# Performance work log

Hardware: AMD Instinct MI355X
Metric: run time of the kernel (lower is better)

Reference implementation:

```python
import jax, jax.numpy as jnp
import numpy as np

VALUE_DIM = 512
VALUE_SIZE = 262144
NUM_LABELS = 64
C = 256
B, T = 4, 1024


def setup_inputs() -> dict:
    key = jax.random.key(0)
    k1, k2, k3, k4, k5 = jax.random.split(key, 5)
    indices = jax.random.randint(k1, (B, T), 0, VALUE_SIZE, dtype=jnp.int64 if jax.config.jax_enable_x64 else jnp.int32)
    scores = jax.random.normal(k2, (B, T), dtype=jnp.float32)
    W = jax.random.normal(k3, (NUM_LABELS, VALUE_DIM, C), dtype=jnp.float32)
    label = jax.random.randint(k4, (B, T), 0, NUM_LABELS, dtype=jnp.int32)
    weight = jax.random.normal(k5, (VALUE_SIZE, VALUE_DIM), dtype=jnp.float32)
    return {"indices": indices, "scores": scores, "W": W, "label": label, "index": 1, "weight": weight}


def reference(indices, scores, W, label, index, weight):
    half = VALUE_DIM // 2
    if index == 1:
        weight_h = weight[:, half:]          # (V, half)
        W_h = W[:, half:, :]                 # (L, half, C)
    else:
        weight_h = weight[:, :half]
        W_h = W[:, :half, :]
    # gather embeddings: (b, t, half)
    selected_values = weight_h[indices]
    # label-indexed matrix gather: (b, t, half, C)
    expanded_params = W_h[label]
    # fused batched matvec + score weighting + sum over t -> (b, C)
    out = jnp.einsum('btd,btdc,bt->bc', selected_values, expanded_params, scores)
    return out
```

## Files before the change

kernel.cpp:

```cpp
#include <hip/hip_runtime.h>

#define Bdim   4
#define Tdim   1024
#define NLAB   64
#define Cdim   256
#define Ddim   512
#define HALF   256
#define BT     (Bdim*Tdim)

__global__ __launch_bounds__(256) void vb_kernel(
    const int*   __restrict__ indices,
    const float* __restrict__ scores,
    const float* __restrict__ W,
    const int*   __restrict__ label,
    const int*   __restrict__ index_p,
    const float* __restrict__ weight,
    float*       __restrict__ out)
{
    const int l     = blockIdx.x & 63;
    const int chunk = blockIdx.x >> 6;
    const int tid   = threadIdx.x;
    const int half  = (index_p[0] == 1) ? HALF : 0;
    const int dglob = half + chunk * 64;

    __shared__ int   s_list[BT];
    __shared__ int   s_count;
    __shared__ float A_part[4][Bdim][64];
    __shared__ float A_red[Bdim][64];
    __shared__ float P[4][Bdim][Cdim];

    if (tid == 0) s_count = 0;
    {
        float* ap = &A_part[0][0][0];
        #pragma unroll
        for (int i = 0; i < 4; ++i) ap[tid + 256 * i] = 0.0f;
    }
    __syncthreads();

    #pragma unroll
    for (int i = 0; i < BT / 256; ++i) {
        int bt = i * 256 + tid;
        if (label[bt] == l) {
            int pos = atomicAdd(&s_count, 1);
            s_list[pos] = bt;
        }
    }
    __syncthreads();
    const int count = s_count;

    const int slot = tid >> 6;
    const int dl   = tid & 63;
    for (int m = slot; m < count; m += 4) {
        int   bt  = s_list[m];
        int   b   = bt >> 10;
        float s   = scores[bt];
        int   idx = indices[bt];
        float w   = weight[(size_t)idx * Ddim + dglob + dl];
        A_part[slot][b][dl] += s * w;
    }
    __syncthreads();

    {
        int b = tid >> 6, d = tid & 63;
        A_red[b][d] = A_part[0][b][d] + A_part[1][b][d]
                    + A_part[2][b][d] + A_part[3][b][d];
    }
    __syncthreads();

    const int c4     = (tid & 63) * 4;
    const int d_base = tid >> 6;

    float4 acc[Bdim];
    #pragma unroll
    for (int b = 0; b < Bdim; ++b) acc[b] = make_float4(0.f, 0.f, 0.f, 0.f);

    #pragma unroll 4
    for (int dd = 0; dd < 16; ++dd) {
        int dloc = dd * 4 + d_base;
        const float4 wv = *(const float4*)(
            W + ((size_t)(l * Ddim + dglob + dloc) * Cdim + c4));
        #pragma unroll
        for (int b = 0; b < Bdim; ++b) {
            float a = A_red[b][dloc];
            acc[b].x += a * wv.x;
            acc[b].y += a * wv.y;
            acc[b].z += a * wv.z;
            acc[b].w += a * wv.w;
        }
    }

    #pragma unroll
    for (int b = 0; b < Bdim; ++b)
        *(float4*)&P[d_base][b][c4] = acc[b];
    __syncthreads();

    {
        int c = tid;
        #pragma unroll
        for (int b = 0; b < Bdim; ++b) {
            float s = P[0][b][c] + P[1][b][c] + P[2][b][c] + P[3][b][c];
            atomicAdd(&out[b * Cdim + c], s);
        }
    }
}

extern "C" void kernel_launch(void* const* d_in, const int* in_sizes, int n_in,
                              void* d_out, int out_size, void* d_ws, size_t ws_size,
                              hipStream_t stream) {
    const int*   indices = (const int*)  d_in[0];
    const float* scores  = (const float*)d_in[1];
    const float* W       = (const float*)d_in[2];
    const int*   label   = (const int*)  d_in[3];
    const int*   index_p = (const int*)  d_in[4];
    const float* weight  = (const float*)d_in[5];
    float*       out     = (float*)d_out;

    hipMemsetAsync(out, 0, (size_t)out_size * sizeof(float), stream);
    vb_kernel<<<dim3(256), dim3(256), 0, stream>>>(
        indices, scores, W, label, index_p, weight, out);
}
```

Before: 608.7 us.

## Vectorize gather into register accumulators and use wave-ballot list compaction

The label scan now reads labels as int4 and compacts matching positions with a wave ballot plus one atomic per wave, replacing per-thread LDS atomics. The gather phase splits each wave into four 16-lane groups that each load a float4 of the embedding row. Each group accumulates all four batch rows in registers instead of doing a read-modify-write to shared memory per element, giving 16 concurrent rows in flight per block. The costs are a 16-way partial reduction in shared memory, more registers, and the W loop being fully unrolled.

```diff
diff --git a/kernel.cpp b/kernel.cpp
--- a/kernel.cpp
+++ b/kernel.cpp
@@ -20,63 +20,86 @@
     const int l     = blockIdx.x & 63;
     const int chunk = blockIdx.x >> 6;
     const int tid   = threadIdx.x;
+    const int lane  = tid & 63;
+    const int wave  = tid >> 6;
     const int half  = (index_p[0] == 1) ? HALF : 0;
     const int dglob = half + chunk * 64;
 
     __shared__ int   s_list[BT];
     __shared__ int   s_count;
-    __shared__ float A_part[4][Bdim][64];
+    __shared__ float A_part[16][Bdim][64];
     __shared__ float A_red[Bdim][64];
     __shared__ float P[4][Bdim][Cdim];
 
     if (tid == 0) s_count = 0;
-    {
-        float* ap = &A_part[0][0][0];
-        #pragma unroll
-        for (int i = 0; i < 4; ++i) ap[tid + 256 * i] = 0.0f;
-    }
     __syncthreads();
 
     #pragma unroll
-    for (int i = 0; i < BT / 256; ++i) {
-        int bt = i * 256 + tid;
-        if (label[bt] == l) {
-            int pos = atomicAdd(&s_count, 1);
-            s_list[pos] = bt;
+    for (int i = 0; i < 4; ++i) {
+        int4 lv = ((const int4*)label)[i * 256 + tid];
+        int bt0 = (i * 256 + tid) * 4;
+        int lv_arr[4] = {lv.x, lv.y, lv.z, lv.w};
+        #pragma unroll
+        for (int j = 0; j < 4; ++j) {
+            bool m = (lv_arr[j] == l);
+            unsigned long long mask = __ballot(m);
+            int base_s = 0;
+            if (lane == 0 && mask)
+                base_s = atomicAdd(&s_count, __popcll(mask));
+            base_s = __shfl(base_s, 0, 64);
+            if (m) {
+                int pre = __popcll(mask & ((1ull << lane) - 1ull));
+                s_list[base_s + pre] = bt0 + j;
+            }
         }
     }
     __syncthreads();
     const int count = s_count;
 
-    const int slot = tid >> 6;
-    const int dl   = tid & 63;
-    for (int m = slot; m < count; m += 4) {
+    const int q    = lane >> 4;
+    const int cl   = lane & 15;
+    const int slot = wave * 4 + q;
+
+    float4 acc0 = {0,0,0,0}, acc1 = {0,0,0,0}, acc2 = {0,0,0,0}, acc3 = {0,0,0,0};
+    for (int m = slot; m < count; m += 16) {
         int   bt  = s_list[m];
         int   b   = bt >> 10;
         float s   = scores[bt];
         int   idx = indices[bt];
-        float w   = weight[(size_t)idx * Ddim + dglob + dl];
-        A_part[slot][b][dl] += s * w;
+        const float4 w = *(const float4*)(weight + (size_t)idx * Ddim + dglob + cl * 4);
+        float s0 = (b == 0) ? s : 0.0f;
+        float s1 = (b == 1) ? s : 0.0f;
+        float s2 = (b == 2) ? s : 0.0f;
+        float s3 = (b == 3) ? s : 0.0f;
+        acc0.x += s0 * w.x; acc0.y += s0 * w.y; acc0.z += s0 * w.z; acc0.w += s0 * w.w;
+        acc1.x += s1 * w.x; acc1.y += s1 * w.y; acc1.z += s1 * w.z; acc1.w += s1 * w.w;
+        acc2.x += s2 * w.x; acc2.y += s2 * w.y; acc2.z += s2 * w.z; acc2.w += s2 * w.w;
+        acc3.x += s3 * w.x; acc3.y += s3 * w.y; acc3.z += s3 * w.z; acc3.w += s3 * w.w;
     }
+    *(float4*)&A_part[slot][0][cl * 4] = acc0;
+    *(float4*)&A_part[slot][1][cl * 4] = acc1;
+    *(float4*)&A_part[slot][2][cl * 4] = acc2;
+    *(float4*)&A_part[slot][3][cl * 4] = acc3;
     __syncthreads();
 
     {
         int b = tid >> 6, d = tid & 63;
-        A_red[b][d] = A_part[0][b][d] + A_part[1][b][d]
-                    + A_part[2][b][d] + A_part[3][b][d];
+        float s = 0.0f;
+        #pragma unroll
+        for (int k = 0; k < 16; ++k) s += A_part[k][b][d];
+        A_red[b][d] = s;
     }
     __syncthreads();
 
-    const int c4     = (tid & 63) * 4;
-    const int d_base = tid >> 6;
+    const int c4 = lane * 4;
 
     float4 acc[Bdim];
     #pragma unroll
     for (int b = 0; b < Bdim; ++b) acc[b] = make_float4(0.f, 0.f, 0.f, 0.f);
 
-    #pragma unroll 4
+    #pragma unroll
     for (int dd = 0; dd < 16; ++dd) {
-        int dloc = dd * 4 + d_base;
+        int dloc = dd * 4 + wave;
         const float4 wv = *(const float4*)(
             W + ((size_t)(l * Ddim + dglob + dloc) * Cdim + c4));
         #pragma unroll
@@ -91,7 +114,7 @@
 
     #pragma unroll
     for (int b = 0; b < Bdim; ++b)
-        *(float4*)&P[d_base][b][c4] = acc[b];
+        *(float4*)&P[wave][b][c4] = acc[b];
     __syncthreads();
 
     {
```

Measured after the change: 604.9 us. About the same (-0.6%).
